# Kernel tuning notes

Measured on AMD Instinct MI355X. Metric: run time of the kernel, lower is better.

The kernel has to match this reference:

```python
import jax, jax.numpy as jnp
import numpy as np
from math import sqrt

D = 512        # output_dim (layer_dims[-1])
H = 4          # num_heads
ATN = D // H   # atn_dim = 128
BERT_D = 768
B = 32         # number of graph pairs
NP = 4096
NH = 4096


def setup_inputs() -> dict:
    key = jax.random.key(0)
    ks = jax.random.split(key, 20)
    inp = {
        'ctx_p': jax.random.normal(ks[0], (NP, D), jnp.float32),
        'ctx_h': jax.random.normal(ks[1], (NH, D), jnp.float32),
        'lhs_p': jax.random.normal(ks[2], (NP, BERT_D), jnp.float32),
        'lhs_h': jax.random.normal(ks[3], (NH, BERT_D), jnp.float32),
        'batch_p': jnp.sort(jax.random.randint(ks[4], (NP,), 0, B)).astype(jnp.int64),
        'batch_h': jnp.sort(jax.random.randint(ks[5], (NH,), 0, B)).astype(jnp.int64),
        # learned parameters (stored [in, out])
        'Wq': jax.random.normal(ks[6], (D, D), jnp.float32) * 0.02,
        'bq': jnp.zeros((D,), jnp.float32),
        'Wk': jax.random.normal(ks[7], (D, D), jnp.float32) * 0.02,
        'bk': jnp.zeros((D,), jnp.float32),
        'Wv': jax.random.normal(ks[8], (BERT_D, BERT_D), jnp.float32) * 0.02,
        'bv': jnp.zeros((BERT_D,), jnp.float32),
        'W1': jax.random.normal(ks[9], (D + BERT_D, 256), jnp.float32) * 0.02,
        'b1': jnp.zeros((256,), jnp.float32),
        'W2': jax.random.normal(ks[10], (256, 128), jnp.float32) * 0.02,
        'ln_g': jnp.ones((128,), jnp.float32),
        'ln_b': jnp.zeros((128,), jnp.float32),
        'Wc': jax.random.normal(ks[11], (128, 3), jnp.float32) * 0.02,
        'bc': jnp.zeros((3,), jnp.float32),
    }
    return inp


def reference(ctx_p, ctx_h, lhs_p, lhs_h, batch_p, batch_h,
              Wq, bq, Wk, bk, Wv, bv, W1, b1, W2, ln_g, ln_b, Wc, bc):
    # q/k projections; torch code does .view(-1, atn_dim, num_heads) -> head is fastest axis
    qs = (ctx_h @ Wq + bq).reshape(-1, ATN, H)          # [nh, atn, H]
    ks = (ctx_p @ Wk + bk).reshape(-1, ATN, H)          # [np, atn, H]
    vs = (lhs_p @ Wv + bv).reshape(-1, H, BERT_D // H)  # [np, H, 768/H]

    atn = jnp.einsum('ndh,mdh->nmh', qs, ks) / sqrt(ATN)  # [nh, np, H]
    # faithful to original: positions where batch ids MATCH are set to -1e10
    mask_same = batch_h[:, None] == batch_p[None, :]       # [nh, np]
    atn = jnp.where(mask_same[:, :, None], jnp.float32(-1e10), atn)
    atn = jax.nn.softmax(atn, axis=1)                      # softmax over premise words m

    attended = jnp.einsum('nmh,mhd->nhd', atn, vs).reshape(-1, BERT_D)  # [nh, 768]

    feats = jnp.concatenate([ctx_h, lhs_h - attended], axis=1)  # [nh, D+768]
    h1 = jax.nn.gelu(feats @ W1 + b1, approximate=False)
    h2 = h1 @ W2                                                # Linear no bias
    mu = h2.mean(axis=-1, keepdims=True)
    var = ((h2 - mu) ** 2).mean(axis=-1, keepdims=True)
    h2 = (h2 - mu) * jax.lax.rsqrt(var + 1e-5) * ln_g + ln_b    # LayerNorm(128)

    # global_mean_pool over batch_h
    pooled = jax.ops.segment_sum(h2, batch_h, num_segments=B)
    counts = jax.ops.segment_sum(jnp.ones((h2.shape[0], 1), h2.dtype), batch_h, num_segments=B)
    pooled = pooled / jnp.maximum(counts, 1.0)

    return pooled @ Wc + bc  # [B, 3]
```

## Files before the change

kernel.cpp:

```cpp
#include <hip/hip_runtime.h>
#include <hip/hip_bf16.h>
#include <math.h>

#define NP_N 4096
#define NH_N 4096
#define D_N 512
#define BERT_N 768
#define H_N 4
#define B_N 32

typedef __attribute__((ext_vector_type(8))) short short8;
typedef __attribute__((ext_vector_type(4))) float f32x4;
typedef __attribute__((ext_vector_type(4))) unsigned short ush4;
typedef unsigned short ushort_t;

__device__ __forceinline__ void gl_lds16(const void* g, void* l) {
    __builtin_amdgcn_global_load_lds((const __attribute__((address_space(1))) void*)g,
                                     (__attribute__((address_space(3))) void*)l, 16, 0, 0);
}
__device__ __forceinline__ void gl_lds4(const void* g, void* l) {
    __builtin_amdgcn_global_load_lds((const __attribute__((address_space(1))) void*)g,
                                     (__attribute__((address_space(3))) void*)l, 4, 0, 0);
}
__device__ __forceinline__ unsigned short f2bu(float f) {
    __hip_bfloat16 b = __float2bfloat16(f);
    return *reinterpret_cast<unsigned short*>(&b);
}
__device__ __forceinline__ float b2f(unsigned short u) {
    union { unsigned int i; float f; } x; x.i = ((unsigned int)u) << 16; return x.f;
}
__device__ __forceinline__ unsigned int pkbf(float a, float b) {
    union { __hip_bfloat162 h; unsigned int u; } x;
    x.h.x = __float2bfloat16(a);
    x.h.y = __float2bfloat16(b);
    return x.u;
}

#define EW_BLOCKS 512
__global__ __launch_bounds__(256) void convert_all(
    const float* __restrict__ ctx_h, const float* __restrict__ ctx_p,
    const float* __restrict__ lhs_p,
    const float* __restrict__ Wq, const float* __restrict__ Wk,
    const float* __restrict__ Wv, const float* __restrict__ W1,
    const float* __restrict__ bq, const float* __restrict__ bk,
    ushort_t* __restrict__ ctxh_bf, ushort_t* __restrict__ ctxp_bf,
    ushort_t* __restrict__ lhsp_bf, ushort_t* __restrict__ feats,
    ushort_t* __restrict__ Wqt, ushort_t* __restrict__ Wkt,
    ushort_t* __restrict__ Wvt, ushort_t* __restrict__ W1t,
    float* __restrict__ bqp, float* __restrict__ bkp)
{
    const int bid = blockIdx.x, t = threadIdx.x;
    if (bid < EW_BLOCKS) {
        const long N0 = 524288, N1 = 1048576, TOT = 1835008;
        for (long i = (long)bid * 256 + t; i < TOT; i += (long)EW_BLOCKS * 256) {
            const float4* src; ush4* dst; long k;
            if (i < N0)      { src = (const float4*)ctx_h; dst = (ush4*)ctxh_bf; k = i; }
            else if (i < N1) { src = (const float4*)ctx_p; dst = (ush4*)ctxp_bf; k = i - N0; }
            else             { src = (const float4*)lhs_p; dst = (ush4*)lhsp_bf; k = i - N1; }
            float4 v = src[k];
            ush4 o; o[0] = f2bu(v.x); o[1] = f2bu(v.y); o[2] = f2bu(v.z); o[3] = f2bu(v.w);
            dst[k] = o;
            if (i < N0) {
                long n = k >> 7, c4 = k & 127;
                ((ush4*)feats)[n * 320 + c4] = o;
            }
        }
        if (bid == 0) {
            for (int n = t; n < 512; n += 256) {
                int np = (n & 3) * 128 + (n >> 2);
                bqp[np] = bq[n];
                bkp[np] = bk[n];
            }
        }
        return;
    }
    int tb = bid - EW_BLOCKS;
    const float* src; ushort_t* dst; int K, N, tile, perm;
    if (tb < 64)       { src = Wq; dst = Wqt; K = 512;  N = 512; tile = tb;       perm = 1; }
    else if (tb < 128) { src = Wk; dst = Wkt; K = 512;  N = 512; tile = tb - 64;  perm = 1; }
    else if (tb < 272) { src = Wv; dst = Wvt; K = 768;  N = 768; tile = tb - 128; perm = 0; }
    else               { src = W1; dst = W1t; K = 1280; N = 256; tile = tb - 272; perm = 0; }
    int ntn = N >> 6;
    int k0 = (tile / ntn) * 64, n0 = (tile % ntn) * 64;
    __shared__ float tl[64][65];
#pragma unroll
    for (int i = 0; i < 16; i++) {
        int idx = t + i * 256; int r = idx >> 6, c = idx & 63;
        tl[r][c] = src[(size_t)(k0 + r) * N + n0 + c];
    }
    __syncthreads();
#pragma unroll
    for (int i = 0; i < 16; i++) {
        int idx = t + i * 256; int r = idx >> 6, c = idx & 63;
        int n = n0 + r;
        int nr = perm ? ((n & 3) * 128 + (n >> 2)) : n;
        dst[(size_t)nr * K + k0 + c] = f2bu(tl[c][r]);
    }
}

template<int BIAS_ROW, int GELU>
__global__ __launch_bounds__(256) void gemm_bf(
    const ushort_t* __restrict__ A, const ushort_t* __restrict__ Bt,
    const float* __restrict__ bias, ushort_t* __restrict__ C,
    int M, int N, int K)
{
    __shared__ ushort_t As[2][64 * 64];
    __shared__ ushort_t Bs[2][64 * 64];
    const int t = threadIdx.x, w = t >> 6, lane = t & 63;
    const int lq = lane & 15, g = lane >> 4;
    const int wm = w >> 1, wn = w & 1;
    const int n0 = blockIdx.x * 64, m0 = blockIdx.y * 64;
    const int nsteps = K >> 6;

    f32x4 acc[2][2];
#pragma unroll
    for (int a = 0; a < 2; a++)
#pragma unroll
        for (int b = 0; b < 2; b++) acc[a][b] = (f32x4){0.f, 0.f, 0.f, 0.f};

    auto STAGE = [&](int buf, int k0) {
#pragma unroll
        for (int jj = 0; jj < 2; jj++) {
            int j = w * 2 + jj;
            int r = j * 8 + (lane >> 3);
            int c = (lane & 7) * 16;
            int cs = c ^ ((r & 7) << 4);
            gl_lds16((const char*)A + ((size_t)(m0 + r) * K + k0) * 2 + cs, (void*)&As[buf][j * 512]);
            gl_lds16((const char*)Bt + ((size_t)(n0 + r) * K + k0) * 2 + cs, (void*)&Bs[buf][j * 512]);
        }
    };

    STAGE(0, 0);
    __syncthreads();
    int cur = 0;
    for (int s = 0; s < nsteps; s++) {
        if (s + 1 < nsteps) STAGE(cur ^ 1, (s + 1) * 64);
        const char* Ab = (const char*)&As[cur][0];
        const char* Bb = (const char*)&Bs[cur][0];
        const int swz = (lq & 7) << 4;
        short8 af[2][2], bf[2][2];
#pragma unroll
        for (int mf = 0; mf < 2; mf++) {
            int r = wm * 32 + mf * 16 + lq;
#pragma unroll
            for (int ks = 0; ks < 2; ks++)
                af[mf][ks] = *(const short8*)(Ab + r * 128 + ((ks * 64 + g * 16) ^ swz));
        }
#pragma unroll
        for (int nf = 0; nf < 2; nf++) {
            int r = wn * 32 + nf * 16 + lq;
#pragma unroll
            for (int ks = 0; ks < 2; ks++)
                bf[nf][ks] = *(const short8*)(Bb + r * 128 + ((ks * 64 + g * 16) ^ swz));
        }
#pragma unroll
        for (int mf = 0; mf < 2; mf++)
#pragma unroll
            for (int nf = 0; nf < 2; nf++)
#pragma unroll
                for (int ks = 0; ks < 2; ks++)
                    acc[mf][nf] = __builtin_amdgcn_mfma_f32_16x16x32_bf16(
                        af[mf][ks], bf[nf][ks], acc[mf][nf], 0, 0, 0);
        __syncthreads();
        cur ^= 1;
    }

#pragma unroll
    for (int mf = 0; mf < 2; mf++) {
#pragma unroll
        for (int nf = 0; nf < 2; nf++) {
            int ncol = n0 + wn * 32 + nf * 16 + lq;
            float bcol = BIAS_ROW ? 0.f : bias[ncol];
#pragma unroll
            for (int j = 0; j < 4; j++) {
                int mrow = m0 + wm * 32 + mf * 16 + 4 * g + j;
                float v = acc[mf][nf][j] + (BIAS_ROW ? bias[mrow] : bcol);
                if (GELU) v = 0.5f * v * (1.f + erff(v * 0.70710678118654752f));
                C[(size_t)mrow * N + ncol] = f2bu(v);
            }
        }
    }
}

__global__ __launch_bounds__(512, 2) void attn_mfma(
    const ushort_t* __restrict__ Qb,
    const ushort_t* __restrict__ Kb,
    const ushort_t* __restrict__ Vtb,
    const int* __restrict__ batch_h, const int* __restrict__ batch_p,
    ushort_t* __restrict__ Opart,
    float* __restrict__ ml)
{
    const int bid = blockIdx.x;
    const int xcd = bid & 7;
    const int h = xcd >> 1;
    const int s = xcd & 1;
    const int n0 = (bid >> 3) * 128;

    __shared__ ushort_t Kt[2][64 * 128];
    __shared__ ushort_t Vt[2][192 * 64];
    __shared__ int bps[2][64];
    __shared__ ushort_t Pl[8][16 * 72];

    const int t = threadIdx.x;
    const int w = t >> 6;
    const int lane = t & 63;
    const int lq = lane & 15;
    const int g = lane >> 4;
    const float scale = 0.08838834764831845f;

    short8 qf[4];
    {
        const ushort_t* qrow = Qb + (size_t)(n0 + w * 16 + lq) * 512 + h * 128;
#pragma unroll
        for (int ks = 0; ks < 4; ks++)
            qf[ks] = *(const short8*)(qrow + ks * 32 + g * 8);
    }
    const int bhq = batch_h[n0 + w * 16 + lq];

    f32x4 Ofr[12];
#pragma unroll
    for (int nt = 0; nt < 12; nt++) Ofr[nt] = (f32x4){0.f, 0.f, 0.f, 0.f};
    float m_run = -1e30f, l_run = 0.f;

    const char* Kg = (const char*)Kb;
    const char* Vg = (const char*)Vtb;
    const int kbase = s * 2048;

    auto STAGE = [&](int buf, int m0k) {
#pragma unroll
        for (int jj = 0; jj < 2; jj++) {
            int j = w * 2 + jj;
            int r = j * 4 + (lane >> 4);
            int c = (lane & 15) * 16;
            gl_lds16(Kg + (size_t)(m0k + r) * 1024 + h * 256 + (c ^ ((r & 7) << 4)),
                     (void*)&Kt[buf][j * 512]);
        }
#pragma unroll
        for (int jj = 0; jj < 3; jj++) {
            int j = w * 3 + jj;
            int r = j * 8 + (lane >> 3);
            int c = (lane & 7) * 16;
            gl_lds16(Vg + ((size_t)(h * 192 + r) * NP_N + m0k) * 2 + (c ^ ((r & 7) << 4)),
                     (void*)&Vt[buf][j * 512]);
        }
        if (w == 0) gl_lds4(batch_p + m0k + lane, (void*)&bps[buf][0]);
    };

    STAGE(0, kbase);
    __syncthreads();
    int cur = 0;

    for (int tile = 0; tile < 32; tile++) {
        if (tile + 1 < 32) STAGE(cur ^ 1, kbase + (tile + 1) * 64);

        f32x4 S[4];
#pragma unroll
        for (int mt = 0; mt < 4; mt++) S[mt] = (f32x4){0.f, 0.f, 0.f, 0.f};
        const char* Kbase = (const char*)&Kt[cur][0];
        const int swz = (lq & 7) << 4;
#pragma unroll
        for (int mt = 0; mt < 4; mt++) {
            int r = mt * 16 + lq;
#pragma unroll
            for (int ks = 0; ks < 4; ks++) {
                short8 kf = *(const short8*)(Kbase + r * 256 + ((ks * 64 + g * 16) ^ swz));
                S[mt] = __builtin_amdgcn_mfma_f32_16x16x32_bf16(kf, qf[ks], S[mt], 0, 0, 0);
            }
        }

        int4 bp4[4];
#pragma unroll
        for (int mt = 0; mt < 4; mt++)
            bp4[mt] = *(const int4*)&bps[cur][16 * mt + 4 * g];

        float mx = -1e30f;
#pragma unroll
        for (int mt = 0; mt < 4; mt++) {
            float v0 = (bp4[mt].x == bhq) ? -1e10f : S[mt][0] * scale;
            float v1 = (bp4[mt].y == bhq) ? -1e10f : S[mt][1] * scale;
            float v2 = (bp4[mt].z == bhq) ? -1e10f : S[mt][2] * scale;
            float v3 = (bp4[mt].w == bhq) ? -1e10f : S[mt][3] * scale;
            S[mt][0] = v0; S[mt][1] = v1; S[mt][2] = v2; S[mt][3] = v3;
            mx = fmaxf(mx, fmaxf(fmaxf(v0, v1), fmaxf(v2, v3)));
        }
        mx = fmaxf(mx, __shfl_xor(mx, 16));
        mx = fmaxf(mx, __shfl_xor(mx, 32));

        float m_new = fmaxf(m_run, mx);
        float rsum = 0.f;
#pragma unroll
        for (int mt = 0; mt < 4; mt++) {
            float e0 = __expf(S[mt][0] - m_new);
            float e1 = __expf(S[mt][1] - m_new);
            float e2 = __expf(S[mt][2] - m_new);
            float e3 = __expf(S[mt][3] - m_new);
            rsum += (e0 + e1) + (e2 + e3);
            uint2 pw;
            pw.x = pkbf(e0, e1);
            pw.y = pkbf(e2, e3);
            *(uint2*)((char*)&Pl[w][0] + lq * 144 + mt * 32 + g * 8) = pw;
        }
        rsum += __shfl_xor(rsum, 16);
        rsum += __shfl_xor(rsum, 32);

        if (__all(mx <= m_run)) {
            l_run += rsum;
        } else {
            float f = __expf(m_run - m_new);
            l_run = l_run * f + rsum;
            m_run = m_new;
            float fr0 = __shfl(f, 4 * g + 0);
            float fr1 = __shfl(f, 4 * g + 1);
            float fr2 = __shfl(f, 4 * g + 2);
            float fr3 = __shfl(f, 4 * g + 3);
#pragma unroll
            for (int nt = 0; nt < 12; nt++) {
                Ofr[nt][0] *= fr0; Ofr[nt][1] *= fr1;
                Ofr[nt][2] *= fr2; Ofr[nt][3] *= fr3;
            }
        }

        const char* Vbase = (const char*)&Vt[cur][0];
#pragma unroll
        for (int ks = 0; ks < 2; ks++) {
            short8 pf = *(const short8*)((const char*)&Pl[w][0] + lq * 144 + ks * 64 + g * 16);
#pragma unroll
            for (int nt = 0; nt < 12; nt++) {
                int vd = nt * 16 + lq;
                short8 vf = *(const short8*)(Vbase + vd * 128 + ((ks * 64 + g * 16) ^ swz));
                Ofr[nt] = __builtin_amdgcn_mfma_f32_16x16x32_bf16(pf, vf, Ofr[nt], 0, 0, 0);
            }
        }

        __syncthreads();
        cur ^= 1;
    }

    const size_t qpl = (size_t)(s * 4 + h) * 4096;
#pragma unroll
    for (int nt = 0; nt < 12; nt++) {
        int vd = nt * 16 + lq;
#pragma unroll
        for (int j = 0; j < 4; j++) {
            int q = n0 + w * 16 + 4 * g + j;
            Opart[(qpl + q) * 192 + vd] = f2bu(Ofr[nt][j]);
        }
    }
    if (lane < 16) {
        int q = n0 + w * 16 + lane;
        ml[(qpl + q) * 2 + 0] = m_run;
        ml[(qpl + q) * 2 + 1] = l_run;
    }
}

__global__ __launch_bounds__(256) void combine_feats(
    const ushort_t* __restrict__ Opart, const float* __restrict__ ml,
    const float* __restrict__ lhs_h, ushort_t* __restrict__ feats)
{
    const int t = threadIdx.x;
#pragma unroll
    for (int i = 0; i < 4; i++) {
        int q = blockIdx.x * 4 + i;
#pragma unroll
        for (int it = 0; it < 3; it++) {
            int c = t + it * 256;
            int h = c / 192, vd = c - h * 192;
            size_t i0 = (size_t)h * 4096 + q;
            size_t i1 = (size_t)(4 + h) * 4096 + q;
            float m0 = ml[i0 * 2], l0 = ml[i0 * 2 + 1];
            float m1 = ml[i1 * 2], l1 = ml[i1 * 2 + 1];
            float m = fmaxf(m0, m1);
            float e0 = __expf(m0 - m), e1 = __expf(m1 - m);
            float linv = 1.f / (l0 * e0 + l1 * e1);
            float O = (b2f(Opart[i0 * 192 + vd]) * e0 + b2f(Opart[i1 * 192 + vd]) * e1) * linv;
            feats[(size_t)q * 1280 + 512 + c] = f2bu(lhs_h[(size_t)q * 768 + c] - O);
        }
    }
}

__global__ __launch_bounds__(256) void h2_ln(
    const ushort_t* __restrict__ h1, const float* __restrict__ W2,
    const float* __restrict__ ln_g, const float* __restrict__ ln_b,
    float* __restrict__ h2out)
{
    const int n0 = blockIdx.x * 8;
    const int t = threadIdx.x;
    __shared__ float h1s[8][256];
    __shared__ float h2s[8][128];

#pragma unroll
    for (int i = 0; i < 8; i++) {
        int idx = t + i * 256; int r = idx >> 8, c = idx & 255;
        h1s[r][c] = b2f(h1[(size_t)(n0 + r) * 256 + c]);
    }
    __syncthreads();

    {
        int o2 = t & 127, gq = t >> 7;
        float acc[4] = {};
        for (int k4 = 0; k4 < 64; k4++) {
            float w0 = W2[(size_t)(k4 * 4 + 0) * 128 + o2];
            float w1 = W2[(size_t)(k4 * 4 + 1) * 128 + o2];
            float w2 = W2[(size_t)(k4 * 4 + 2) * 128 + o2];
            float w3 = W2[(size_t)(k4 * 4 + 3) * 128 + o2];
#pragma unroll
            for (int q = 0; q < 4; q++) {
                float4 hh = *(const float4*)&h1s[gq * 4 + q][k4 * 4];
                acc[q] += hh.x * w0 + hh.y * w1 + hh.z * w2 + hh.w * w3;
            }
        }
#pragma unroll
        for (int q = 0; q < 4; q++) h2s[gq * 4 + q][o2] = acc[q];
    }
    __syncthreads();

    {
        int wv = t >> 6, lane = t & 63;
#pragma unroll
        for (int s = 0; s < 2; s++) {
            int nd = wv * 2 + s;
            float x0 = h2s[nd][lane], x1 = h2s[nd][lane + 64];
            float sum = x0 + x1;
#pragma unroll
            for (int off = 32; off; off >>= 1) sum += __shfl_xor(sum, off);
            float mu = sum * (1.f / 128.f);
            float d0 = x0 - mu, d1 = x1 - mu;
            float s2 = d0 * d0 + d1 * d1;
#pragma unroll
            for (int off = 32; off; off >>= 1) s2 += __shfl_xor(s2, off);
            float rstd = rsqrtf(s2 * (1.f / 128.f) + 1e-5f);
            size_t base = (size_t)(n0 + nd) * 128;
            h2out[base + lane]      = d0 * rstd * ln_g[lane] + ln_b[lane];
            h2out[base + lane + 64] = d1 * rstd * ln_g[lane + 64] + ln_b[lane + 64];
        }
    }
}

__global__ void ranges_kernel(const int* __restrict__ bh, int* __restrict__ lo,
                              int Nn, int Bn)
{
    int n = blockIdx.x * blockDim.x + threadIdx.x;
    if (n >= Nn) return;
    int b = bh[n];
    int prev = (n == 0) ? -1 : bh[n - 1];
    for (int bb = prev + 1; bb <= b; bb++) lo[bb] = n;
    if (n == Nn - 1) for (int bb = b + 1; bb <= Bn; bb++) lo[bb] = Nn;
}

__global__ __launch_bounds__(128) void pool_cls(
    const float* __restrict__ h2, const int* __restrict__ lo,
    const float* __restrict__ Wc, const float* __restrict__ bc,
    float* __restrict__ out)
{
    int b = blockIdx.x, t = threadIdx.x;
    int s = lo[b], e = lo[b + 1];
    float acc = 0.f;
    for (int n = s; n < e; n++) acc += h2[(size_t)n * 128 + t];
    float pooled = acc / fmaxf((float)(e - s), 1.f);
    __shared__ float red[128];
    for (int c = 0; c < 3; c++) {
        red[t] = pooled * Wc[t * 3 + c];
        __syncthreads();
        for (int off = 64; off > 0; off >>= 1) {
            if (t < off) red[t] += red[t + off];
            __syncthreads();
        }
        if (t == 0) out[b * 3 + c] = red[0] + bc[c];
        __syncthreads();
    }
}

extern "C" void kernel_launch(void* const* d_in, const int* in_sizes, int n_in,
                              void* d_out, int out_size, void* d_ws, size_t ws_size,
                              hipStream_t stream)
{
    const float* ctx_p  = (const float*)d_in[0];
    const float* ctx_h  = (const float*)d_in[1];
    const float* lhs_p  = (const float*)d_in[2];
    const float* lhs_h  = (const float*)d_in[3];
    const int*   batch_p = (const int*)d_in[4];
    const int*   batch_h = (const int*)d_in[5];
    const float* Wq = (const float*)d_in[6];
    const float* bq = (const float*)d_in[7];
    const float* Wk = (const float*)d_in[8];
    const float* bk = (const float*)d_in[9];
    const float* Wv = (const float*)d_in[10];
    const float* bv = (const float*)d_in[11];
    const float* W1 = (const float*)d_in[12];
    const float* b1 = (const float*)d_in[13];
    const float* W2 = (const float*)d_in[14];
    const float* ln_g = (const float*)d_in[15];
    const float* ln_b = (const float*)d_in[16];
    const float* Wc = (const float*)d_in[17];
    const float* bc = (const float*)d_in[18];
    float* out = (float*)d_out;

    ushort_t* u = (ushort_t*)d_ws;
    ushort_t* ctxh_bf = u;
    ushort_t* ctxp_bf = ctxh_bf + 2097152;
    ushort_t* lhsp_bf = ctxp_bf + 2097152;
    ushort_t* Opart   = ctxh_bf;
    ushort_t* Wqt  = lhsp_bf + 3145728;
    ushort_t* Wkt  = Wqt + 262144;
    ushort_t* Wvt  = Wkt + 262144;
    ushort_t* W1t  = Wvt + 589824;
    ushort_t* Qb   = W1t + 327680;
    ushort_t* Kb   = Qb + 2097152;
    ushort_t* Vtb  = Kb + 2097152;
    ushort_t* feats = Vtb + 3145728;
    ushort_t* h1   = feats + 5242880;
    float* fbase = (float*)(h1 + 1048576);
    float* ml   = fbase;
    float* h2   = ml + 131072;
    float* bqp  = h2 + 524288;
    float* bkp  = bqp + 512;
    int*   lo   = (int*)(bkp + 512);

    convert_all<<<864, 256, 0, stream>>>(
        ctx_h, ctx_p, lhs_p, Wq, Wk, Wv, W1, bq, bk,
        ctxh_bf, ctxp_bf, lhsp_bf, feats, Wqt, Wkt, Wvt, W1t, bqp, bkp);

    gemm_bf<0, 0><<<dim3(8, 64), 256, 0, stream>>>(ctxh_bf, Wqt, bqp, Qb, NH_N, 512, 512);
    gemm_bf<0, 0><<<dim3(8, 64), 256, 0, stream>>>(ctxp_bf, Wkt, bkp, Kb, NP_N, 512, 512);
    gemm_bf<1, 0><<<dim3(64, 12), 256, 0, stream>>>(Wvt, lhsp_bf, bv, Vtb, 768, NP_N, 768);

    attn_mfma<<<256, 512, 0, stream>>>(Qb, Kb, Vtb, batch_h, batch_p, Opart, ml);

    combine_feats<<<1024, 256, 0, stream>>>(Opart, ml, lhs_h, feats);

    gemm_bf<0, 1><<<dim3(4, 64), 256, 0, stream>>>(feats, W1t, b1, h1, NH_N, 256, 1280);

    h2_ln<<<512, 256, 0, stream>>>(h1, W2, ln_g, ln_b, h2);
    ranges_kernel<<<16, 256, 0, stream>>>(batch_h, lo, NH_N, B_N);
    pool_cls<<<B_N, 128, 0, stream>>>(h2, lo, Wc, bc, out);
}
```

Measured before the change: 194.4 us.

## Restructure attention: 32 queries per wave, intra-block key split, exp2 lazy rescale

Each wave now processes two 16-query groups, so every K and V fragment read from LDS feeds two MFMAs. The two halves of the block's 2048-key range go to two groups of four waves, and their partial results are merged in LDS at the end. Softmax uses exp2 with a pre-multiplied scale and skips rescaling the output unless the running max grows by more than 8. The P tile reuses the current K buffer, and batch_p is now read from global memory. Separately, the ctx_h bf16 copy is dropped: the Q GEMM reads directly from the feats buffer using a new lda stride. The cost is higher register pressure, an extra block-wide barrier per tile, and close to 160KB of LDS per block.

```diff
diff --git a/kernel.cpp b/kernel.cpp
--- a/kernel.cpp
+++ b/kernel.cpp
@@ -17,10 +17,6 @@
 __device__ __forceinline__ void gl_lds16(const void* g, void* l) {
     __builtin_amdgcn_global_load_lds((const __attribute__((address_space(1))) void*)g,
                                      (__attribute__((address_space(3))) void*)l, 16, 0, 0);
-}
-__device__ __forceinline__ void gl_lds4(const void* g, void* l) {
-    __builtin_amdgcn_global_load_lds((const __attribute__((address_space(1))) void*)g,
-                                     (__attribute__((address_space(3))) void*)l, 4, 0, 0);
 }
 __device__ __forceinline__ unsigned short f2bu(float f) {
     __hip_bfloat16 b = __float2bfloat16(f);
@@ -43,8 +39,8 @@
     const float* __restrict__ Wq, const float* __restrict__ Wk,
     const float* __restrict__ Wv, const float* __restrict__ W1,
     const float* __restrict__ bq, const float* __restrict__ bk,
-    ushort_t* __restrict__ ctxh_bf, ushort_t* __restrict__ ctxp_bf,
-    ushort_t* __restrict__ lhsp_bf, ushort_t* __restrict__ feats,
+    ushort_t* __restrict__ ctxp_bf, ushort_t* __restrict__ lhsp_bf,
+    ushort_t* __restrict__ feats,
     ushort_t* __restrict__ Wqt, ushort_t* __restrict__ Wkt,
     ushort_t* __restrict__ Wvt, ushort_t* __restrict__ W1t,
     float* __restrict__ bqp, float* __restrict__ bkp)
@@ -53,16 +49,23 @@
     if (bid < EW_BLOCKS) {
         const long N0 = 524288, N1 = 1048576, TOT = 1835008;
         for (long i = (long)bid * 256 + t; i < TOT; i += (long)EW_BLOCKS * 256) {
-            const float4* src; ush4* dst; long k;
-            if (i < N0)      { src = (const float4*)ctx_h; dst = (ush4*)ctxh_bf; k = i; }
-            else if (i < N1) { src = (const float4*)ctx_p; dst = (ush4*)ctxp_bf; k = i - N0; }
-            else             { src = (const float4*)lhs_p; dst = (ush4*)lhsp_bf; k = i - N1; }
-            float4 v = src[k];
-            ush4 o; o[0] = f2bu(v.x); o[1] = f2bu(v.y); o[2] = f2bu(v.z); o[3] = f2bu(v.w);
-            dst[k] = o;
+            float4 v; ush4 o;
             if (i < N0) {
+                long k = i;
+                v = ((const float4*)ctx_h)[k];
+                o[0] = f2bu(v.x); o[1] = f2bu(v.y); o[2] = f2bu(v.z); o[3] = f2bu(v.w);
                 long n = k >> 7, c4 = k & 127;
                 ((ush4*)feats)[n * 320 + c4] = o;
+            } else if (i < N1) {
+                long k = i - N0;
+                v = ((const float4*)ctx_p)[k];
+                o[0] = f2bu(v.x); o[1] = f2bu(v.y); o[2] = f2bu(v.z); o[3] = f2bu(v.w);
+                ((ush4*)ctxp_bf)[k] = o;
+            } else {
+                long k = i - N1;
+                v = ((const float4*)lhs_p)[k];
+                o[0] = f2bu(v.x); o[1] = f2bu(v.y); o[2] = f2bu(v.z); o[3] = f2bu(v.w);
+                ((ush4*)lhsp_bf)[k] = o;
             }
         }
         if (bid == 0) {
@@ -100,7 +103,7 @@
 
 template<int BIAS_ROW, int GELU>
 __global__ __launch_bounds__(256) void gemm_bf(
-    const ushort_t* __restrict__ A, const ushort_t* __restrict__ Bt,
+    const ushort_t* __restrict__ A, int lda, const ushort_t* __restrict__ Bt,
     const float* __restrict__ bias, ushort_t* __restrict__ C,
     int M, int N, int K)
 {
@@ -125,7 +128,7 @@
             int r = j * 8 + (lane >> 3);
             int c = (lane & 7) * 16;
             int cs = c ^ ((r & 7) << 4);
-            gl_lds16((const char*)A + ((size_t)(m0 + r) * K + k0) * 2 + cs, (void*)&As[buf][j * 512]);
+            gl_lds16((const char*)A + ((size_t)(m0 + r) * lda + k0) * 2 + cs, (void*)&As[buf][j * 512]);
             gl_lds16((const char*)Bt + ((size_t)(n0 + r) * K + k0) * 2 + cs, (void*)&Bs[buf][j * 512]);
         }
     };
@@ -191,144 +194,166 @@
     float* __restrict__ ml)
 {
     const int bid = blockIdx.x;
-    const int xcd = bid & 7;
-    const int h = xcd >> 1;
-    const int s = xcd & 1;
+    const int h = (bid & 7) >> 1;
+    const int s = bid & 1;
     const int n0 = (bid >> 3) * 128;
 
-    __shared__ ushort_t Kt[2][64 * 128];
-    __shared__ ushort_t Vt[2][192 * 64];
-    __shared__ int bps[2][64];
-    __shared__ ushort_t Pl[8][16 * 72];
+    __shared__ __align__(16) char smem[163840];
 
     const int t = threadIdx.x;
-    const int w = t >> 6;
-    const int lane = t & 63;
-    const int lq = lane & 15;
-    const int g = lane >> 4;
-    const float scale = 0.08838834764831845f;
-
-    short8 qf[4];
-    {
-        const ushort_t* qrow = Qb + (size_t)(n0 + w * 16 + lq) * 512 + h * 128;
+    const int w = t >> 6, o = w >> 2, wq = w & 3;
+    const int lane = t & 63, lq = lane & 15, g = lane >> 4;
+    const int lqm = (lq & 7) << 4;
+    const float scl2 = 0.12754245006257576f;
+
+    char* Kt0 = smem + (o * 2 + 0) * 16384;
+    char* Kt1 = smem + (o * 2 + 1) * 16384;
+    char* Vt0 = smem + 65536 + (o * 2 + 0) * 24576;
+    char* Vt1 = smem + 65536 + (o * 2 + 1) * 24576;
+
+    short8 qf[2][4];
+    int bhq[2];
+#pragma unroll
+    for (int qg = 0; qg < 2; qg++) {
+        const ushort_t* qrow = Qb + (size_t)(n0 + wq * 32 + qg * 16 + lq) * 512 + h * 128;
 #pragma unroll
         for (int ks = 0; ks < 4; ks++)
-            qf[ks] = *(const short8*)(qrow + ks * 32 + g * 8);
-    }
-    const int bhq = batch_h[n0 + w * 16 + lq];
-
-    f32x4 Ofr[12];
-#pragma unroll
-    for (int nt = 0; nt < 12; nt++) Ofr[nt] = (f32x4){0.f, 0.f, 0.f, 0.f};
-    float m_run = -1e30f, l_run = 0.f;
+            qf[qg][ks] = *(const short8*)(qrow + ks * 32 + g * 8);
+        bhq[qg] = batch_h[n0 + wq * 32 + qg * 16 + lq];
+    }
+
+    f32x4 Ofr[2][12];
+#pragma unroll
+    for (int qg = 0; qg < 2; qg++)
+#pragma unroll
+        for (int nt = 0; nt < 12; nt++) Ofr[qg][nt] = (f32x4){0.f, 0.f, 0.f, 0.f};
+    float m_run[2] = {-1e30f, -1e30f}, l_run[2] = {0.f, 0.f};
 
     const char* Kg = (const char*)Kb;
     const char* Vg = (const char*)Vtb;
-    const int kbase = s * 2048;
-
-    auto STAGE = [&](int buf, int m0k) {
-#pragma unroll
-        for (int jj = 0; jj < 2; jj++) {
-            int j = w * 2 + jj;
+    const int kb = s * 2048 + o * 1024;
+
+    auto STAGE = [&](char* Kd, char* Vd, int m0k) {
+#pragma unroll
+        for (int jj = 0; jj < 4; jj++) {
+            int j = wq * 4 + jj;
             int r = j * 4 + (lane >> 4);
             int c = (lane & 15) * 16;
             gl_lds16(Kg + (size_t)(m0k + r) * 1024 + h * 256 + (c ^ ((r & 7) << 4)),
-                     (void*)&Kt[buf][j * 512]);
-        }
-#pragma unroll
-        for (int jj = 0; jj < 3; jj++) {
-            int j = w * 3 + jj;
+                     Kd + j * 1024);
+        }
+#pragma unroll
+        for (int jj = 0; jj < 6; jj++) {
+            int j = wq * 6 + jj;
             int r = j * 8 + (lane >> 3);
             int c = (lane & 7) * 16;
-            gl_lds16(Vg + ((size_t)(h * 192 + r) * NP_N + m0k) * 2 + (c ^ ((r & 7) << 4)),
-                     (void*)&Vt[buf][j * 512]);
-        }
-        if (w == 0) gl_lds4(batch_p + m0k + lane, (void*)&bps[buf][0]);
+            gl_lds16(Vg + ((size_t)(h * 192 + r) * 4096 + m0k) * 2 + (c ^ ((r & 7) << 4)),
+                     Vd + j * 1024);
+        }
     };
 
-    STAGE(0, kbase);
+    STAGE(Kt0, Vt0, kb);
     __syncthreads();
     int cur = 0;
 
-    for (int tile = 0; tile < 32; tile++) {
-        if (tile + 1 < 32) STAGE(cur ^ 1, kbase + (tile + 1) * 64);
-
-        f32x4 S[4];
-#pragma unroll
-        for (int mt = 0; mt < 4; mt++) S[mt] = (f32x4){0.f, 0.f, 0.f, 0.f};
-        const char* Kbase = (const char*)&Kt[cur][0];
-        const int swz = (lq & 7) << 4;
+    for (int tile = 0; tile < 16; tile++) {
+        char* Kc = cur ? Kt1 : Kt0;
+        char* Vc = cur ? Vt1 : Vt0;
+        if (tile + 1 < 16) STAGE(cur ? Kt0 : Kt1, cur ? Vt0 : Vt1, kb + (tile + 1) * 64);
+
+        f32x4 S[2][4];
+#pragma unroll
+        for (int qg = 0; qg < 2; qg++)
+#pragma unroll
+            for (int mt = 0; mt < 4; mt++) S[qg][mt] = (f32x4){0.f, 0.f, 0.f, 0.f};
 #pragma unroll
         for (int mt = 0; mt < 4; mt++) {
-            int r = mt * 16 + lq;
+            const char* rbase = Kc + (mt * 16 + lq) * 256;
 #pragma unroll
             for (int ks = 0; ks < 4; ks++) {
-                short8 kf = *(const short8*)(Kbase + r * 256 + ((ks * 64 + g * 16) ^ swz));
-                S[mt] = __builtin_amdgcn_mfma_f32_16x16x32_bf16(kf, qf[ks], S[mt], 0, 0, 0);
+                short8 kf = *(const short8*)(rbase + ((ks * 64 + g * 16) ^ lqm));
+                S[0][mt] = __builtin_amdgcn_mfma_f32_16x16x32_bf16(kf, qf[0][ks], S[0][mt], 0, 0, 0);
+                S[1][mt] = __builtin_amdgcn_mfma_f32_16x16x32_bf16(kf, qf[1][ks], S[1][mt], 0, 0, 0);
             }
         }
 
         int4 bp4[4];
 #pragma unroll
         for (int mt = 0; mt < 4; mt++)
-            bp4[mt] = *(const int4*)&bps[cur][16 * mt + 4 * g];
-
-        float mx = -1e30f;
-#pragma unroll
-        for (int mt = 0; mt < 4; mt++) {
-            float v0 = (bp4[mt].x == bhq) ? -1e10f : S[mt][0] * scale;
-            float v1 = (bp4[mt].y == bhq) ? -1e10f : S[mt][1] * scale;
-            float v2 = (bp4[mt].z == bhq) ? -1e10f : S[mt][2] * scale;
-            float v3 = (bp4[mt].w == bhq) ? -1e10f : S[mt][3] * scale;
-            S[mt][0] = v0; S[mt][1] = v1; S[mt][2] = v2; S[mt][3] = v3;
-            mx = fmaxf(mx, fmaxf(fmaxf(v0, v1), fmaxf(v2, v3)));
-        }
-        mx = fmaxf(mx, __shfl_xor(mx, 16));
-        mx = fmaxf(mx, __shfl_xor(mx, 32));
-
-        float m_new = fmaxf(m_run, mx);
-        float rsum = 0.f;
-#pragma unroll
-        for (int mt = 0; mt < 4; mt++) {
-            float e0 = __expf(S[mt][0] - m_new);
-            float e1 = __expf(S[mt][1] - m_new);
-            float e2 = __expf(S[mt][2] - m_new);
-            float e3 = __expf(S[mt][3] - m_new);
-            rsum += (e0 + e1) + (e2 + e3);
-            uint2 pw;
-            pw.x = pkbf(e0, e1);
-            pw.y = pkbf(e2, e3);
-            *(uint2*)((char*)&Pl[w][0] + lq * 144 + mt * 32 + g * 8) = pw;
-        }
-        rsum += __shfl_xor(rsum, 16);
-        rsum += __shfl_xor(rsum, 32);
-
-        if (__all(mx <= m_run)) {
-            l_run += rsum;
-        } else {
-            float f = __expf(m_run - m_new);
-            l_run = l_run * f + rsum;
-            m_run = m_new;
-            float fr0 = __shfl(f, 4 * g + 0);
-            float fr1 = __shfl(f, 4 * g + 1);
-            float fr2 = __shfl(f, 4 * g + 2);
-            float fr3 = __shfl(f, 4 * g + 3);
+            bp4[mt] = *(const int4*)&batch_p[kb + tile * 64 + mt * 16 + 4 * g];
+
+        float mx[2];
+#pragma unroll
+        for (int qg = 0; qg < 2; qg++) {
+            float m = -1e30f;
+#pragma unroll
+            for (int mt = 0; mt < 4; mt++) {
+                float v0 = (bp4[mt].x == bhq[qg]) ? -1e9f : S[qg][mt][0] * scl2;
+                float v1 = (bp4[mt].y == bhq[qg]) ? -1e9f : S[qg][mt][1] * scl2;
+                float v2 = (bp4[mt].z == bhq[qg]) ? -1e9f : S[qg][mt][2] * scl2;
+                float v3 = (bp4[mt].w == bhq[qg]) ? -1e9f : S[qg][mt][3] * scl2;
+                S[qg][mt][0] = v0; S[qg][mt][1] = v1; S[qg][mt][2] = v2; S[qg][mt][3] = v3;
+                m = fmaxf(m, fmaxf(fmaxf(v0, v1), fmaxf(v2, v3)));
+            }
+            m = fmaxf(m, __shfl_xor(m, 16));
+            m = fmaxf(m, __shfl_xor(m, 32));
+            mx[qg] = m;
+        }
+        bool ng = __all((mx[0] <= m_run[0] + 8.f) && (mx[1] <= m_run[1] + 8.f));
+
+        uint2 P2[2][4];
+#pragma unroll
+        for (int qg = 0; qg < 2; qg++) {
+            float m_new = ng ? m_run[qg] : fmaxf(m_run[qg], mx[qg]);
+            float rsum = 0.f;
+#pragma unroll
+            for (int mt = 0; mt < 4; mt++) {
+                float e0 = exp2f(S[qg][mt][0] - m_new);
+                float e1 = exp2f(S[qg][mt][1] - m_new);
+                float e2 = exp2f(S[qg][mt][2] - m_new);
+                float e3 = exp2f(S[qg][mt][3] - m_new);
+                rsum += (e0 + e1) + (e2 + e3);
+                P2[qg][mt].x = pkbf(e0, e1);
+                P2[qg][mt].y = pkbf(e2, e3);
+            }
+            rsum += __shfl_xor(rsum, 16);
+            rsum += __shfl_xor(rsum, 32);
+            if (ng) {
+                l_run[qg] += rsum;
+            } else {
+                float f = exp2f(m_run[qg] - m_new);
+                l_run[qg] = l_run[qg] * f + rsum;
+                m_run[qg] = m_new;
+                float fr0 = __shfl(f, 4 * g + 0);
+                float fr1 = __shfl(f, 4 * g + 1);
+                float fr2 = __shfl(f, 4 * g + 2);
+                float fr3 = __shfl(f, 4 * g + 3);
+#pragma unroll
+                for (int nt = 0; nt < 12; nt++) {
+                    Ofr[qg][nt][0] *= fr0; Ofr[qg][nt][1] *= fr1;
+                    Ofr[qg][nt][2] *= fr2; Ofr[qg][nt][3] *= fr3;
+                }
+            }
+        }
+
+        __syncthreads();
+
+        char* Pz = Kc + wq * 4096;
+#pragma unroll
+        for (int qg = 0; qg < 2; qg++)
+#pragma unroll
+            for (int mt = 0; mt < 4; mt++)
+                *(uint2*)(Pz + qg * 2048 + lq * 128 + ((mt * 32 + g * 8) ^ lqm)) = P2[qg][mt];
+
+#pragma unroll
+        for (int ks = 0; ks < 2; ks++) {
+            short8 pf0 = *(const short8*)(Pz + 0 * 2048 + lq * 128 + ((ks * 64 + g * 16) ^ lqm));
+            short8 pf1 = *(const short8*)(Pz + 1 * 2048 + lq * 128 + ((ks * 64 + g * 16) ^ lqm));
 #pragma unroll
             for (int nt = 0; nt < 12; nt++) {
-                Ofr[nt][0] *= fr0; Ofr[nt][1] *= fr1;
-                Ofr[nt][2] *= fr2; Ofr[nt][3] *= fr3;
-            }
-        }
-
-        const char* Vbase = (const char*)&Vt[cur][0];
-#pragma unroll
-        for (int ks = 0; ks < 2; ks++) {
-            short8 pf = *(const short8*)((const char*)&Pl[w][0] + lq * 144 + ks * 64 + g * 16);
-#pragma unroll
-            for (int nt = 0; nt < 12; nt++) {
-                int vd = nt * 16 + lq;
-                short8 vf = *(const short8*)(Vbase + vd * 128 + ((ks * 64 + g * 16) ^ swz));
-                Ofr[nt] = __builtin_amdgcn_mfma_f32_16x16x32_bf16(pf, vf, Ofr[nt], 0, 0, 0);
+                short8 vf = *(const short8*)(Vc + (nt * 16 + lq) * 128 + ((ks * 64 + g * 16) ^ lqm));
+                Ofr[0][nt] = __builtin_amdgcn_mfma_f32_16x16x32_bf16(pf0, vf, Ofr[0][nt], 0, 0, 0);
+                Ofr[1][nt] = __builtin_amdgcn_mfma_f32_16x16x32_bf16(pf1, vf, Ofr[1][nt], 0, 0, 0);
             }
         }
 
@@ -336,20 +361,52 @@
         cur ^= 1;
     }
 
-    const size_t qpl = (size_t)(s * 4 + h) * 4096;
-#pragma unroll
-    for (int nt = 0; nt < 12; nt++) {
-        int vd = nt * 16 + lq;
-#pragma unroll
-        for (int j = 0; j < 4; j++) {
-            int q = n0 + w * 16 + 4 * g + j;
-            Opart[(qpl + q) * 192 + vd] = f2bu(Ofr[nt][j]);
-        }
-    }
-    if (lane < 16) {
-        int q = n0 + w * 16 + lane;
-        ml[(qpl + q) * 2 + 0] = m_run;
-        ml[(qpl + q) * 2 + 1] = l_run;
+    const int tq = wq * 64 + lane;
+    float* mOf = (float*)smem;
+    float* mls = (float*)(smem + 98304);
+    if (o == 1) {
+#pragma unroll
+        for (int qg = 0; qg < 2; qg++) {
+#pragma unroll
+            for (int nt = 0; nt < 12; nt++)
+                *(f32x4*)(mOf + tq * 96 + qg * 48 + nt * 4) = Ofr[qg][nt];
+            if (g == 0) {
+                mls[(wq * 16 + lq) * 4 + qg * 2 + 0] = m_run[qg];
+                mls[(wq * 16 + lq) * 4 + qg * 2 + 1] = l_run[qg];
+            }
+        }
+    }
+    __syncthreads();
+    if (o == 0) {
+        const size_t plane = (size_t)(s * 4 + h) * 4096;
+#pragma unroll
+        for (int qg = 0; qg < 2; qg++) {
+            float m1 = mls[(wq * 16 + lq) * 4 + qg * 2 + 0];
+            float l1 = mls[(wq * 16 + lq) * 4 + qg * 2 + 1];
+            float m = fmaxf(m_run[qg], m1);
+            float a0 = exp2f(m_run[qg] - m), a1 = exp2f(m1 - m);
+            float l = l_run[qg] * a0 + l1 * a1;
+            int qrow = n0 + wq * 32 + qg * 16;
+            if (g == 0) {
+                ml[(plane + qrow + lq) * 2 + 0] = m;
+                ml[(plane + qrow + lq) * 2 + 1] = l;
+            }
+            float f0[4], f1[4];
+#pragma unroll
+            for (int j = 0; j < 4; j++) {
+                f0[j] = __shfl(a0, 4 * g + j);
+                f1[j] = __shfl(a1, 4 * g + j);
+            }
+#pragma unroll
+            for (int nt = 0; nt < 12; nt++) {
+                f32x4 o1 = *(f32x4*)(mOf + tq * 96 + qg * 48 + nt * 4);
+#pragma unroll
+                for (int j = 0; j < 4; j++) {
+                    float val = Ofr[qg][nt][j] * f0[j] + o1[j] * f1[j];
+                    Opart[(plane + qrow + 4 * g + j) * 192 + nt * 16 + lq] = f2bu(val);
+                }
+            }
+        }
     }
 }
 
@@ -370,7 +427,7 @@
             float m0 = ml[i0 * 2], l0 = ml[i0 * 2 + 1];
             float m1 = ml[i1 * 2], l1 = ml[i1 * 2 + 1];
             float m = fmaxf(m0, m1);
-            float e0 = __expf(m0 - m), e1 = __expf(m1 - m);
+            float e0 = exp2f(m0 - m), e1 = exp2f(m1 - m);
             float linv = 1.f / (l0 * e0 + l1 * e1);
             float O = (b2f(Opart[i0 * 192 + vd]) * e0 + b2f(Opart[i1 * 192 + vd]) * e1) * linv;
             feats[(size_t)q * 1280 + 512 + c] = f2bu(lhs_h[(size_t)q * 768 + c] - O);
@@ -417,8 +474,8 @@
     {
         int wv = t >> 6, lane = t & 63;
 #pragma unroll
-        for (int s = 0; s < 2; s++) {
-            int nd = wv * 2 + s;
+        for (int sx = 0; sx < 2; sx++) {
+            int nd = wv * 2 + sx;
             float x0 = h2s[nd][lane], x1 = h2s[nd][lane + 64];
             float sum = x0 + x1;
 #pragma unroll
@@ -496,39 +553,37 @@
     float* out = (float*)d_out;
 
     ushort_t* u = (ushort_t*)d_ws;
-    ushort_t* ctxh_bf = u;
-    ushort_t* ctxp_bf = ctxh_bf + 2097152;
+    ushort_t* ctxp_bf = u;
     ushort_t* lhsp_bf = ctxp_bf + 2097152;
-    ushort_t* Opart   = ctxh_bf;
     ushort_t* Wqt  = lhsp_bf + 3145728;
     ushort_t* Wkt  = Wqt + 262144;
     ushort_t* Wvt  = Wkt + 262144;
+    ushort_t* Opart = u;
     ushort_t* W1t  = Wvt + 589824;
     ushort_t* Qb   = W1t + 327680;
     ushort_t* Kb   = Qb + 2097152;
     ushort_t* Vtb  = Kb + 2097152;
     ushort_t* feats = Vtb + 3145728;
     ushort_t* h1   = feats + 5242880;
-    float* fbase = (float*)(h1 + 1048576);
-    float* ml   = fbase;
-    float* h2   = ml + 131072;
-    float* bqp  = h2 + 524288;
-    float* bkp  = bqp + 512;
-    int*   lo   = (int*)(bkp + 512);
+    float* ml  = (float*)(h1 + 1048576);
+    float* h2  = ml + 65536;
+    float* bqp = h2 + 524288;
+    float* bkp = bqp + 512;
+    int*   lo  = (int*)(bkp + 512);
 
     convert_all<<<864, 256, 0, stream>>>(
         ctx_h, ctx_p, lhs_p, Wq, Wk, Wv, W1, bq, bk,
-        ctxh_bf, ctxp_bf, lhsp_bf, feats, Wqt, Wkt, Wvt, W1t, bqp, bkp);
-
-    gemm_bf<0, 0><<<dim3(8, 64), 256, 0, stream>>>(ctxh_bf, Wqt, bqp, Qb, NH_N, 512, 512);
-    gemm_bf<0, 0><<<dim3(8, 64), 256, 0, stream>>>(ctxp_bf, Wkt, bkp, Kb, NP_N, 512, 512);
-    gemm_bf<1, 0><<<dim3(64, 12), 256, 0, stream>>>(Wvt, lhsp_bf, bv, Vtb, 768, NP_N, 768);
+        ctxp_bf, lhsp_bf, feats, Wqt, Wkt, Wvt, W1t, bqp, bkp);
+
+    gemm_bf<0, 0><<<dim3(8, 64), 256, 0, stream>>>(feats, 1280, Wqt, bqp, Qb, NH_N, 512, 512);
+    gemm_bf<0, 0><<<dim3(8, 64), 256, 0, stream>>>(ctxp_bf, 512, Wkt, bkp, Kb, NP_N, 512, 512);
+    gemm_bf<1, 0><<<dim3(64, 12), 256, 0, stream>>>(Wvt, 768, lhsp_bf, bv, Vtb, 768, NP_N, 768);
 
     attn_mfma<<<256, 512, 0, stream>>>(Qb, Kb, Vtb, batch_h, batch_p, Opart, ml);
 
     combine_feats<<<1024, 256, 0, stream>>>(Opart, ml, lhs_h, feats);
 
-    gemm_bf<0, 1><<<dim3(4, 64), 256, 0, stream>>>(feats, W1t, b1, h1, NH_N, 256, 1280);
+    gemm_bf<0, 1><<<dim3(4, 64), 256, 0, stream>>>(feats, 1280, W1t, b1, h1, NH_N, 256, 1280);
 
     h2_ln<<<512, 256, 0, stream>>>(h1, W2, ln_g, ln_b, h2);
     ranges_kernel<<<16, 256, 0, stream>>>(batch_h, lo, NH_N, B_N);
```

New measurement: 195.0 us. About the same (+0.3%).
